# Kernel optimization log

Measured on AMD Instinct MI355X. Metric: run time of the kernel, lower is better.

Reference implementation:

```python
import jax, jax.numpy as jnp
import numpy as np

B, KB, SEQ, HID = 8, 16, 512, 768  # batch, two_times_batch, max_length, hidden
NEG_INF = float('-inf')


def _l2_normalize(x, eps=1e-12):
    # torch F.normalize: x / max(||x||_2, eps)
    n = jnp.sqrt(jnp.sum(x * x, axis=-1, keepdims=True))
    return x / jnp.maximum(n, eps)


def setup_inputs() -> dict:
    key = jax.random.key(0)
    k1, k2, k3, k4 = jax.random.split(key, 4)
    return {
        'query_embs': jax.random.normal(k1, (B, SEQ, HID), dtype=jnp.float32),
        'key_embs': jax.random.normal(k2, (KB, SEQ, HID), dtype=jnp.float32),
        'alpha_raw': jnp.float32(0.1),  # learnable scalar, cfg.model.alpha init
        'q_mask': jax.random.randint(k3, (B, SEQ), 0, 2, dtype=jnp.int32),
        'k_mask': jax.random.randint(k4, (KB, SEQ), 0, 2, dtype=jnp.int32),
    }


def reference(query_embs, key_embs, alpha_raw, q_mask, k_mask):
    # cfg: distance_weightning='exp', use_softmax=True, gumbel_temp=None
    qn = _l2_normalize(query_embs)          # [B, S, H]
    kn = _l2_normalize(key_embs)            # [KB, T, H]

    # cosine similarity: [B, KB, S, T]
    sim = jnp.einsum('ish,jth->ijst', qn, kn)

    # exp distance weighting, alpha = leaky_relu(alpha_raw)
    alpha = jax.nn.leaky_relu(alpha_raw)
    pos = jnp.arange(SEQ, dtype=jnp.float32)
    distance = jnp.abs(pos[:, None] - pos[None, :])        # [S, T]
    sim = sim * jnp.exp(-alpha * distance)

    valid = (q_mask[:, None, :, None] != 0) & (k_mask[None, :, None, :] != 0)
    logits = jnp.where(valid, sim, NEG_INF)

    p = jax.nn.softmax(logits, axis=-1)                    # [B, KB, S, T]
    p = jnp.nan_to_num(p, nan=0.0)

    # aggregate normalized keys under attention, dot with queries
    aggregated = jnp.einsum('ijst,jth->ijsh', p, kn)       # [B, KB, S, H]
    scores = jnp.einsum('ish,ijsh->ijs', qn, aggregated)   # [B, KB, S]
    scores = scores * q_mask[:, None, :].astype(scores.dtype)
    return scores.sum(axis=-1)                             # [B, KB]
```

## Files before the change

### kernel.cpp

```cpp
#include <hip/hip_runtime.h>
#include <stdint.h>

#define B_   8
#define KB_  16
#define SEQ_ 512
#define HID_ 768

#define NKB  (HID_ / 32)
#define QRB  (B_  * SEQ_ / 16)
#define KRB  (KB_ * SEQ_ / 16)

typedef __attribute__((ext_vector_type(4))) _Float16 half4;
typedef __attribute__((ext_vector_type(8))) _Float16 half8;
typedef __attribute__((ext_vector_type(4))) float    floatx4;

#define GLOBAL_AS __attribute__((address_space(1)))
#define LDS_AS    __attribute__((address_space(3)))

static __device__ __forceinline__ void async_tile16(const _Float16* g, _Float16* l)
{
    __builtin_amdgcn_global_load_lds((const GLOBAL_AS uint32_t*)g,
                                     (LDS_AS uint32_t*)l, 16, 0, 0);
}

#define LP 776

__global__ __launch_bounds__(256)
void prep_tile(const float* __restrict__ Q, const float* __restrict__ K,
               _Float16* __restrict__ Qt, _Float16* __restrict__ Kt)
{
    const int rb = blockIdx.x;
    const float* src;
    _Float16*    dst;
    if (rb < QRB) { src = Q + (size_t)rb * 16 * HID_;          dst = Qt + (size_t)rb * NKB * 512; }
    else          { src = K + (size_t)(rb - QRB) * 16 * HID_;  dst = Kt + (size_t)(rb - QRB) * NKB * 512; }

    __shared__ _Float16 Ls[16 * LP];
    const int wave = threadIdx.x >> 6;
    const int lane = threadIdx.x & 63;

#pragma unroll
    for (int rr = 0; rr < 4; ++rr) {
        int row = wave * 4 + rr;
        const float* s = src + (size_t)row * HID_;
        float4 v[3];
        float ss = 0.f;
#pragma unroll
        for (int it = 0; it < 3; ++it) {
            v[it] = *(const float4*)(s + lane * 4 + it * 256);
            ss += v[it].x * v[it].x + v[it].y * v[it].y + v[it].z * v[it].z + v[it].w * v[it].w;
        }
#pragma unroll
        for (int m = 1; m < 64; m <<= 1) ss += __shfl_xor(ss, m, 64);
        float sc = 1.0f / fmaxf(sqrtf(ss), 1e-12f);
#pragma unroll
        for (int it = 0; it < 3; ++it) {
            half4 h = { (_Float16)(v[it].x * sc), (_Float16)(v[it].y * sc),
                        (_Float16)(v[it].z * sc), (_Float16)(v[it].w * sc) };
            *(half4*)(Ls + row * LP + lane * 4 + it * 256) = h;
        }
    }
    __syncthreads();

#pragma unroll
    for (int rep = 0; rep < 6; ++rep) {
        int slot = rep * 256 + threadIdx.x;
        int kb   = slot >> 6;
        int ln   = slot & 63;
        int row  = ln & 15;
        int ko   = kb * 32 + (ln >> 4) * 8;
        half8 h = *(const half8*)(Ls + row * LP + ko);
        *(half8*)(dst + (size_t)kb * 512 + (size_t)ln * 8) = h;
    }
}

__global__ __launch_bounds__(512, 4)
void li_part(const _Float16* __restrict__ Qt, const _Float16* __restrict__ Kt,
             const float* __restrict__ alpha_p, const int* __restrict__ kmask,
             float* __restrict__ Pbuf)
{
    const int st = blockIdx.x >> 1;
    const int tb = blockIdx.x & 1;
    const int j  = blockIdx.y;
    const int i  = blockIdx.z;

    const int tid  = threadIdx.x;
    const int lane = tid & 63;
    const int wave = tid >> 6;
    const int quad = lane >> 4;
    const int l16  = lane & 15;
    const int wr   = wave >> 2;
    const int wc   = wave & 3;

    __shared__ _Float16 Sbuf[3][24 * 512];
    __shared__ float lred[4][128], nred[4][128];

    const int qbase = i * 32 + st * 8;
    const int kbase = j * 32 + tb * 16;

    const _Float16* gsrc[3];
    _Float16*       ldst0[3];
#pragma unroll
    for (int q = 0; q < 3; ++q) {
        int t   = wave * 3 + q;
        int rbg = (t < 8) ? (qbase + t) : (kbase + (t - 8));
        const _Float16* base = (t < 8) ? Qt : Kt;
        gsrc[q]  = base + (size_t)rbg * NKB * 512 + (size_t)lane * 8;
        ldst0[q] = &Sbuf[0][t * 512];
    }

    floatx4 acc[4][4];
#pragma unroll
    for (int rt = 0; rt < 4; ++rt)
#pragma unroll
        for (int ct = 0; ct < 4; ++ct)
            acc[rt][ct] = (floatx4){0.f, 0.f, 0.f, 0.f};

#pragma unroll
    for (int q = 0; q < 3; ++q)
        async_tile16(gsrc[q], ldst0[q]);
#pragma unroll
    for (int q = 0; q < 3; ++q)
        async_tile16(gsrc[q] + 512, ldst0[q] + 24 * 512);

    for (int kb = 0; kb < NKB; ++kb) {
        const int slot = kb % 3;

        __builtin_amdgcn_sched_barrier(0);
        asm volatile("s_barrier" ::: "memory");
        __builtin_amdgcn_sched_barrier(0);

        if (kb + 2 < NKB) {
            const int ps = (kb + 2) % 3;
#pragma unroll
            for (int q = 0; q < 3; ++q)
                async_tile16(gsrc[q] + (size_t)(kb + 2) * 512, ldst0[q] + ps * (24 * 512));
            asm volatile("s_waitcnt vmcnt(6)\n\ts_barrier" ::: "memory");
        } else if (kb + 1 < NKB) {
            asm volatile("s_waitcnt vmcnt(3)\n\ts_barrier" ::: "memory");
        } else {
            asm volatile("s_waitcnt vmcnt(0)\n\ts_barrier" ::: "memory");
        }
        __builtin_amdgcn_sched_barrier(0);

        const _Float16* Qs = &Sbuf[slot][0];
        const _Float16* Ks = &Sbuf[slot][8 * 512];
        half8 af[4], bf[4];
#pragma unroll
        for (int rt = 0; rt < 4; ++rt)
            af[rt] = *(const half8*)(Qs + (wr * 4 + rt) * 512 + lane * 8);
#pragma unroll
        for (int ct = 0; ct < 4; ++ct)
            bf[ct] = *(const half8*)(Ks + (wc * 4 + ct) * 512 + lane * 8);

        __builtin_amdgcn_s_setprio(1);
#pragma unroll
        for (int rt = 0; rt < 4; ++rt)
#pragma unroll
            for (int ct = 0; ct < 4; ++ct)
                acc[rt][ct] = __builtin_amdgcn_mfma_f32_16x16x32_f16(af[rt], bf[ct], acc[rt][ct], 0, 0, 0);
        __builtin_amdgcn_s_setprio(0);
    }

    const float araw  = *alpha_p;
    const float alpha = araw >= 0.f ? araw : 0.01f * araw;

    const int* km = kmask + j * SEQ_ + tb * 256;
    int kmv[4]; float tgf[4];
#pragma unroll
    for (int ct = 0; ct < 4; ++ct) {
        int t_loc = wc * 64 + ct * 16 + l16;
        kmv[ct] = km[t_loc];
        tgf[ct] = (float)(tb * 256 + t_loc);
    }
#pragma unroll
    for (int rt = 0; rt < 4; ++rt) {
#pragma unroll
        for (int r = 0; r < 4; ++r) {
            float sgf = (float)(st * 128 + wr * 64 + rt * 16 + quad * 4 + r);
            float ps = 0.f, ns = 0.f;
#pragma unroll
            for (int ct = 0; ct < 4; ++ct) {
                float cv = acc[rt][ct][r];
                float e  = kmv[ct] ? __expf(cv * __expf(-alpha * fabsf(sgf - tgf[ct]))) : 0.f;
                ps += e;
                ns += e * cv;
            }
#pragma unroll
            for (int msk = 1; msk < 16; msk <<= 1) {
                ps += __shfl_xor(ps, msk, 64);
                ns += __shfl_xor(ns, msk, 64);
            }
            if (l16 == 0) {
                int rloc = wr * 64 + rt * 16 + quad * 4 + r;
                lred[wc][rloc] = ps;
                nred[wc][rloc] = ns;
            }
        }
    }
    __syncthreads();

    if (tid < 128) {
        float l = lred[0][tid] + lred[1][tid] + lred[2][tid] + lred[3][tid];
        float n = nred[0][tid] + nred[1][tid] + nred[2][tid] + nred[3][tid];
        size_t base = (((size_t)(i * KB_ + j) * SEQ_) + st * 128 + tid) * 4 + tb * 2;
        Pbuf[base]     = l;
        Pbuf[base + 1] = n;
    }
}

__global__ __launch_bounds__(256)
void li_reduce(const float* __restrict__ Pbuf, const int* __restrict__ qmask,
               float* __restrict__ out)
{
    const int ij = blockIdx.x;
    const int i  = ij >> 4;
    const int tid = threadIdx.x;
    __shared__ float red[4];

    float sum = 0.f;
#pragma unroll
    for (int rep = 0; rep < 2; ++rep) {
        int s = tid + rep * 256;
        float4 a = *(const float4*)(Pbuf + ((size_t)ij * SEQ_ + s) * 4);
        float l = a.x + a.z;
        float n = a.y + a.w;
        float sc = (l > 0.f) ? n / l : 0.f;
        if (qmask[i * SEQ_ + s] == 0) sc = 0.f;
        sum += sc;
    }
#pragma unroll
    for (int m = 1; m < 64; m <<= 1) sum += __shfl_xor(sum, m, 64);
    if ((tid & 63) == 0) red[tid >> 6] = sum;
    __syncthreads();
    if (tid == 0) out[ij] = red[0] + red[1] + red[2] + red[3];
}

extern "C" void kernel_launch(void* const* d_in, const int* in_sizes, int n_in,
                              void* d_out, int out_size, void* d_ws, size_t ws_size,
                              hipStream_t stream)
{
    const float* Q       = (const float*)d_in[0];
    const float* K       = (const float*)d_in[1];
    const float* alpha_p = (const float*)d_in[2];
    const int*   qmask   = (const int*)d_in[3];
    const int*   kmask   = (const int*)d_in[4];
    float*       out     = (float*)d_out;

    char* ws = (char*)d_ws;
    _Float16* Qt   = (_Float16*)ws;
    _Float16* Kt   = (_Float16*)(ws + (size_t)B_ * SEQ_ * HID_ * 2);
    float*    Pbuf = (float*)   (ws + (size_t)(B_ + KB_) * SEQ_ * HID_ * 2);

    prep_tile<<<QRB + KRB, 256, 0, stream>>>(Q, K, Qt, Kt);

    dim3 grid(8, KB_, B_);
    li_part<<<grid, 512, 0, stream>>>(Qt, Kt, alpha_p, kmask, Pbuf);

    li_reduce<<<B_ * KB_, 256, 0, stream>>>(Pbuf, qmask, out);
}
```

Measured before the change: 146.6 us.

## Double query tile per block and split k-step into two phased MFMA halves

```diff
diff --git a/kernel.cpp b/kernel.cpp
--- a/kernel.cpp
+++ b/kernel.cpp
@@ -74,15 +74,15 @@
     }
 }
 
-__global__ __launch_bounds__(512, 4)
+__global__ __launch_bounds__(512, 2)
 void li_part(const _Float16* __restrict__ Qt, const _Float16* __restrict__ Kt,
              const float* __restrict__ alpha_p, const int* __restrict__ kmask,
              float* __restrict__ Pbuf)
 {
-    const int st = blockIdx.x >> 1;
-    const int tb = blockIdx.x & 1;
-    const int j  = blockIdx.y;
-    const int i  = blockIdx.z;
+    const int st2 = blockIdx.x >> 1;
+    const int tb  = blockIdx.x & 1;
+    const int j   = blockIdx.y;
+    const int i   = blockIdx.z;
 
     const int tid  = threadIdx.x;
     const int lane = tid & 63;
@@ -92,74 +92,94 @@
     const int wr   = wave >> 2;
     const int wc   = wave & 3;
 
-    __shared__ _Float16 Sbuf[3][24 * 512];
-    __shared__ float lred[4][128], nred[4][128];
-
-    const int qbase = i * 32 + st * 8;
+    __shared__ _Float16 Sbuf[3][32 * 512];
+    __shared__ float lred[4][256], nred[4][256];
+
+    const int qbase = i * 32 + st2 * 16;
     const int kbase = j * 32 + tb * 16;
 
-    const _Float16* gsrc[3];
-    _Float16*       ldst0[3];
-#pragma unroll
-    for (int q = 0; q < 3; ++q) {
-        int t   = wave * 3 + q;
-        int rbg = (t < 8) ? (qbase + t) : (kbase + (t - 8));
-        const _Float16* base = (t < 8) ? Qt : Kt;
-        gsrc[q]  = base + (size_t)rbg * NKB * 512 + (size_t)lane * 8;
-        ldst0[q] = &Sbuf[0][t * 512];
-    }
-
-    floatx4 acc[4][4];
-#pragma unroll
-    for (int rt = 0; rt < 4; ++rt)
+    const _Float16* gA0 = Qt + (size_t)(qbase + wave)     * (NKB * 512) + (size_t)lane * 8;
+    const _Float16* gA1 = Qt + (size_t)(qbase + 8 + wave) * (NKB * 512) + (size_t)lane * 8;
+    const _Float16* gB0 = Kt + (size_t)(kbase + wave)     * (NKB * 512) + (size_t)lane * 8;
+    const _Float16* gB1 = Kt + (size_t)(kbase + 8 + wave) * (NKB * 512) + (size_t)lane * 8;
+
+    floatx4 acc[8][4];
+#pragma unroll
+    for (int rt = 0; rt < 8; ++rt)
 #pragma unroll
         for (int ct = 0; ct < 4; ++ct)
             acc[rt][ct] = (floatx4){0.f, 0.f, 0.f, 0.f};
 
 #pragma unroll
-    for (int q = 0; q < 3; ++q)
-        async_tile16(gsrc[q], ldst0[q]);
-#pragma unroll
-    for (int q = 0; q < 3; ++q)
-        async_tile16(gsrc[q] + 512, ldst0[q] + 24 * 512);
-
-    for (int kb = 0; kb < NKB; ++kb) {
-        const int slot = kb % 3;
-
-        __builtin_amdgcn_sched_barrier(0);
-        asm volatile("s_barrier" ::: "memory");
-        __builtin_amdgcn_sched_barrier(0);
-
-        if (kb + 2 < NKB) {
-            const int ps = (kb + 2) % 3;
-#pragma unroll
-            for (int q = 0; q < 3; ++q)
-                async_tile16(gsrc[q] + (size_t)(kb + 2) * 512, ldst0[q] + ps * (24 * 512));
-            asm volatile("s_waitcnt vmcnt(6)\n\ts_barrier" ::: "memory");
-        } else if (kb + 1 < NKB) {
-            asm volatile("s_waitcnt vmcnt(3)\n\ts_barrier" ::: "memory");
-        } else {
-            asm volatile("s_waitcnt vmcnt(0)\n\ts_barrier" ::: "memory");
-        }
-        __builtin_amdgcn_sched_barrier(0);
-
-        const _Float16* Qs = &Sbuf[slot][0];
-        const _Float16* Ks = &Sbuf[slot][8 * 512];
-        half8 af[4], bf[4];
-#pragma unroll
-        for (int rt = 0; rt < 4; ++rt)
-            af[rt] = *(const half8*)(Qs + (wr * 4 + rt) * 512 + lane * 8);
+    for (int t = 0; t < 2; ++t) {
+        _Float16* Lb = &Sbuf[t][0];
+        async_tile16(gA0 + t * 512, Lb + (wave)      * 512);
+        async_tile16(gA1 + t * 512, Lb + (8 + wave)  * 512);
+        async_tile16(gB0 + t * 512, Lb + (16 + wave) * 512);
+        async_tile16(gB1 + t * 512, Lb + (24 + wave) * 512);
+    }
+    asm volatile("s_waitcnt vmcnt(4)\n\ts_barrier" ::: "memory");
+    __builtin_amdgcn_sched_barrier(0);
+
+    for (int t = 0; t < NKB; ++t) {
+        const _Float16* Rb = &Sbuf[t % 3][0];
+        _Float16*       Wb = &Sbuf[(t + 2) % 3][0];
+
+        half8 bf[4], af[4];
 #pragma unroll
         for (int ct = 0; ct < 4; ++ct)
-            bf[ct] = *(const half8*)(Ks + (wc * 4 + ct) * 512 + lane * 8);
+            bf[ct] = *(const half8*)(Rb + (16 + wc * 4 + ct) * 512 + lane * 8);
+#pragma unroll
+        for (int rq = 0; rq < 4; ++rq)
+            af[rq] = *(const half8*)(Rb + (wr * 8 + rq) * 512 + lane * 8);
+
+        if (t + 2 < NKB) {
+            async_tile16(gA0 + (size_t)(t + 2) * 512, Wb + (wave)     * 512);
+            async_tile16(gA1 + (size_t)(t + 2) * 512, Wb + (8 + wave) * 512);
+        }
+        __builtin_amdgcn_sched_barrier(0);
+        asm volatile("s_barrier" ::: "memory");
+        __builtin_amdgcn_sched_barrier(0);
+        asm volatile("s_waitcnt lgkmcnt(0)" ::: "memory");
+        __builtin_amdgcn_sched_barrier(0);
 
         __builtin_amdgcn_s_setprio(1);
 #pragma unroll
-        for (int rt = 0; rt < 4; ++rt)
+        for (int rq = 0; rq < 4; ++rq)
 #pragma unroll
             for (int ct = 0; ct < 4; ++ct)
-                acc[rt][ct] = __builtin_amdgcn_mfma_f32_16x16x32_f16(af[rt], bf[ct], acc[rt][ct], 0, 0, 0);
+                acc[rq][ct] = __builtin_amdgcn_mfma_f32_16x16x32_f16(af[rq], bf[ct], acc[rq][ct], 0, 0, 0);
         __builtin_amdgcn_s_setprio(0);
+        __builtin_amdgcn_sched_barrier(0);
+        asm volatile("s_barrier" ::: "memory");
+        __builtin_amdgcn_sched_barrier(0);
+
+#pragma unroll
+        for (int rq = 0; rq < 4; ++rq)
+            af[rq] = *(const half8*)(Rb + (wr * 8 + 4 + rq) * 512 + lane * 8);
+
+        if (t + 2 < NKB) {
+            async_tile16(gB0 + (size_t)(t + 2) * 512, Wb + (16 + wave) * 512);
+            async_tile16(gB1 + (size_t)(t + 2) * 512, Wb + (24 + wave) * 512);
+        }
+        if (t + 2 < NKB) asm volatile("s_waitcnt vmcnt(4)" ::: "memory");
+        else             asm volatile("s_waitcnt vmcnt(0)" ::: "memory");
+        __builtin_amdgcn_sched_barrier(0);
+        asm volatile("s_barrier" ::: "memory");
+        __builtin_amdgcn_sched_barrier(0);
+        asm volatile("s_waitcnt lgkmcnt(0)" ::: "memory");
+        __builtin_amdgcn_sched_barrier(0);
+
+        __builtin_amdgcn_s_setprio(1);
+#pragma unroll
+        for (int rq = 0; rq < 4; ++rq)
+#pragma unroll
+            for (int ct = 0; ct < 4; ++ct)
+                acc[4 + rq][ct] = __builtin_amdgcn_mfma_f32_16x16x32_f16(af[rq], bf[ct], acc[4 + rq][ct], 0, 0, 0);
+        __builtin_amdgcn_s_setprio(0);
+        __builtin_amdgcn_sched_barrier(0);
+        asm volatile("s_barrier" ::: "memory");
+        __builtin_amdgcn_sched_barrier(0);
     }
 
     const float araw  = *alpha_p;
@@ -174,10 +194,10 @@
         tgf[ct] = (float)(tb * 256 + t_loc);
     }
 #pragma unroll
-    for (int rt = 0; rt < 4; ++rt) {
+    for (int rt = 0; rt < 8; ++rt) {
 #pragma unroll
         for (int r = 0; r < 4; ++r) {
-            float sgf = (float)(st * 128 + wr * 64 + rt * 16 + quad * 4 + r);
+            float sgf = (float)(st2 * 256 + wr * 128 + rt * 16 + quad * 4 + r);
             float ps = 0.f, ns = 0.f;
 #pragma unroll
             for (int ct = 0; ct < 4; ++ct) {
@@ -192,7 +212,7 @@
                 ns += __shfl_xor(ns, msk, 64);
             }
             if (l16 == 0) {
-                int rloc = wr * 64 + rt * 16 + quad * 4 + r;
+                int rloc = wr * 128 + rt * 16 + quad * 4 + r;
                 lred[wc][rloc] = ps;
                 nred[wc][rloc] = ns;
             }
@@ -200,10 +220,10 @@
     }
     __syncthreads();
 
-    if (tid < 128) {
+    if (tid < 256) {
         float l = lred[0][tid] + lred[1][tid] + lred[2][tid] + lred[3][tid];
         float n = nred[0][tid] + nred[1][tid] + nred[2][tid] + nred[3][tid];
-        size_t base = (((size_t)(i * KB_ + j) * SEQ_) + st * 128 + tid) * 4 + tb * 2;
+        size_t base = (((size_t)(i * KB_ + j) * SEQ_) + st2 * 256 + tid) * 4 + tb * 2;
         Pbuf[base]     = l;
         Pbuf[base + 1] = n;
     }
@@ -254,7 +274,7 @@
 
     prep_tile<<<QRB + KRB, 256, 0, stream>>>(Q, K, Qt, Kt);
 
-    dim3 grid(8, KB_, B_);
+    dim3 grid(4, KB_, B_);
     li_part<<<grid, 512, 0, stream>>>(Qt, Kt, alpha_p, kmask, Pbuf);
 
     li_reduce<<<B_ * KB_, 256, 0, stream>>>(Pbuf, qmask, out);
```

Measured after the change: 154.5 us. +5.4%, slower.
